# Performance work log

Measured on AMD Instinct MI355X. Metric: run time of the kernel, lower is better.

Reference implementation:

```python
import jax, jax.numpy as jnp
import numpy as np


def setup_inputs() -> dict:
    key = jax.random.key(0)
    kq, kk, kv, km, kb = jax.random.split(key, 5)
    B, H, S, D = 4, 16, 2048, 64
    Q = jax.random.normal(kq, (B, H, S, D), dtype=jnp.float32)
    K = jax.random.normal(kk, (B, H, S, D), dtype=jnp.float32)
    V = jax.random.normal(kv, (B, H, S, D), dtype=jnp.float32)
    # key-padding style mask, broadcasts over query dim; 0 -> masked
    mask = jax.random.randint(km, (B, 1, 1, S), 0, 2, dtype=jnp.int32)
    attn_bias = jax.random.normal(kb, (1, H, S, S), dtype=jnp.float32)
    return {"Q": Q, "K": K, "V": V, "mask": mask, "attn_bias": attn_bias}


def reference(Q, K, V, mask, attn_bias):
    d_k = Q.shape[-1]
    scale = 1.0 / jnp.sqrt(jnp.asarray(d_k, Q.dtype))
    # [B,H,Sq,Sk] scores
    scores = jnp.einsum("bhqd,bhkd->bhqk", Q, K) * scale
    scores = scores + attn_bias
    scores = jnp.where(mask == 0, jnp.asarray(-1e9, scores.dtype), scores)
    attn = jax.nn.softmax(scores, axis=-1)
    # dropout is identity in eval/reference mode
    output = jnp.einsum("bhqk,bhkd->bhqd", attn, V)
    return output, attn
```

## Files before the change

### kernel.cpp

```cpp
#include <hip/hip_runtime.h>

#define NB 4
#define NH 16
#define NS 2048
#define ND 64
#define PST 2052

typedef __attribute__((ext_vector_type(8))) short short8;
typedef __attribute__((ext_vector_type(4))) short short4v;
typedef __attribute__((ext_vector_type(4))) float floatx4;
typedef __attribute__((ext_vector_type(2))) float floatx2;

__device__ __forceinline__ unsigned short f2bf(float f) {
  unsigned u = __builtin_bit_cast(unsigned, f);
  u = (u + 0x7FFFu + ((u >> 16) & 1u)) >> 16;
  return (unsigned short)u;
}
__device__ __forceinline__ float bf2f(unsigned short s) {
  unsigned u = ((unsigned)s) << 16;
  return __builtin_bit_cast(float, u);
}

__global__ __launch_bounds__(256) void prep_k_kernel(const float* __restrict__ K,
                                                     unsigned short* __restrict__ kb) {
  size_t i = ((size_t)blockIdx.x * 256 + threadIdx.x) * 4;
  floatx4 v = *(const floatx4*)(K + i);
  unsigned long long o = 0;
  o |= (unsigned long long)f2bf(v[0]);
  o |= (unsigned long long)f2bf(v[1]) << 16;
  o |= (unsigned long long)f2bf(v[2]) << 32;
  o |= (unsigned long long)f2bf(v[3]) << 48;
  *(unsigned long long*)(kb + i) = o;
}

__global__ __launch_bounds__(256) void prep_vt_kernel(const float* __restrict__ V,
                                                      unsigned short* __restrict__ vt) {
  __shared__ float tile[64][65];
  int kc = blockIdx.x & 31;
  int bh = blockIdx.x >> 5;
  int k0 = kc * 64;
  const float* src = V + ((size_t)bh * NS + k0) * ND;
  int t = threadIdx.x;
  int r0 = t >> 4;
  int c = (t & 15) * 4;
  for (int rr = 0; rr < 4; ++rr) {
    int r = rr * 16 + r0;
    floatx4 v = *(const floatx4*)(src + (size_t)r * ND + c);
    tile[r][c + 0] = v[0]; tile[r][c + 1] = v[1];
    tile[r][c + 2] = v[2]; tile[r][c + 3] = v[3];
  }
  __syncthreads();
  unsigned short* dst = vt + (size_t)bh * ND * NS + k0;
  for (int i = 0; i < 16; ++i) {
    int lin = i * 256 + t;
    int d = lin >> 6, k = lin & 63;
    dst[(size_t)d * NS + k] = f2bf(tile[k][d]);
  }
}

__global__ __launch_bounds__(1024, 8) void attn_kernel(
    const float* __restrict__ Q,
    const unsigned short* __restrict__ Kb,
    const unsigned short* __restrict__ VT,
    const int* __restrict__ mask,
    const float* __restrict__ bias,
    float* __restrict__ out,
    float* __restrict__ attn) {
  extern __shared__ char smem[];
  unsigned short* P = (unsigned short*)smem;
  float* sums = (float*)(smem + 16 * PST * 2);

  const int bid = blockIdx.x;
  const int b = bid & 3;
  const int qt = (bid >> 2) & 127;
  const int h = bid >> 9;
  const int q0 = qt * 16;

  const int tid = threadIdx.x;
  const int wave = tid >> 6;
  const int lane = tid & 63;
  const int lg = lane >> 4;
  const int lc = lane & 15;
  const int lg4 = lg * 4;
  const int lg8 = lg * 8;

  const size_t bh = (size_t)(b * NH + h);

  short8 aq[2];
  {
    const float* qrow = Q + (bh * NS + (size_t)(q0 + lc)) * ND + lg8;
#pragma unroll
    for (int t = 0; t < 2; ++t) {
      floatx4 f0 = *(const floatx4*)(qrow + t * 32);
      floatx4 f1 = *(const floatx4*)(qrow + t * 32 + 4);
      short8 a;
      a[0] = (short)f2bf(f0[0]); a[1] = (short)f2bf(f0[1]);
      a[2] = (short)f2bf(f0[2]); a[3] = (short)f2bf(f0[3]);
      a[4] = (short)f2bf(f1[0]); a[5] = (short)f2bf(f1[1]);
      a[6] = (short)f2bf(f1[2]); a[7] = (short)f2bf(f1[3]);
      aq[t] = a;
    }
  }

  const unsigned short* kp = Kb + bh * NS * ND + (size_t)lc * ND + lg8;
  const float* bprow = bias + ((size_t)h * NS + (size_t)(q0 + lg4)) * NS + lc;
  const int* mp = mask + b * NS + lc;

  float psum[4] = {0.f, 0.f, 0.f, 0.f};
  const int kb0 = wave * 128;

  short8 kfa[2], kfb[2];
  float bvv[2][4];
  int mvv[2];
  {
    const int k0 = kb0;
    kfa[0] = *(const short8*)(kp + (size_t)k0 * ND);
    kfb[0] = *(const short8*)(kp + (size_t)k0 * ND + 32);
    mvv[0] = mp[k0];
#pragma unroll
    for (int r = 0; r < 4; ++r) bvv[0][r] = bprow[(size_t)r * NS + k0];
  }
#pragma unroll
  for (int it = 0; it < 8; ++it) {
    const int cur = it & 1, nxt = cur ^ 1;
    if (it < 7) {
      const int k1 = kb0 + (it + 1) * 16;
      kfa[nxt] = *(const short8*)(kp + (size_t)k1 * ND);
      kfb[nxt] = *(const short8*)(kp + (size_t)k1 * ND + 32);
      mvv[nxt] = mp[k1];
#pragma unroll
      for (int r = 0; r < 4; ++r) bvv[nxt][r] = bprow[(size_t)r * NS + k1];
    }
    const int k0 = kb0 + it * 16;
    floatx4 c = {0.f, 0.f, 0.f, 0.f};
    c = __builtin_amdgcn_mfma_f32_16x16x32_bf16(aq[0], kfa[cur], c, 0, 0, 0);
    c = __builtin_amdgcn_mfma_f32_16x16x32_bf16(aq[1], kfb[cur], c, 0, 0, 0);
#pragma unroll
    for (int r = 0; r < 4; ++r) {
      float s = c[r] * 0.125f + bvv[cur][r];
      float p = mvv[cur] ? __expf(s) : 0.f;
      psum[r] += p;
      P[(lg4 + r) * PST + k0 + lc] = f2bf(p);
    }
  }

#pragma unroll
  for (int r = 0; r < 4; ++r) {
    float v = psum[r];
    v += __shfl_xor(v, 1);
    v += __shfl_xor(v, 2);
    v += __shfl_xor(v, 4);
    v += __shfl_xor(v, 8);
    if (lc == 0) sums[wave * 16 + lg4 + r] = v;
  }
  __syncthreads();

  {
    const int row = wave;
    float tot = 0.f;
#pragma unroll
    for (int w = 0; w < 16; ++w) tot += sums[w * 16 + row];
    const float inv = 1.f / tot;
    float* arow = attn + (bh * NS + (size_t)(q0 + row)) * NS;
    const unsigned short* prow = P + row * PST;
#pragma unroll
    for (int it = 0; it < 8; ++it) {
      const int col = it * 256 + lane * 4;
      short4v pv = *(const short4v*)(prow + col);
      floatx4 f;
      f[0] = bf2f((unsigned short)pv[0]) * inv;
      f[1] = bf2f((unsigned short)pv[1]) * inv;
      f[2] = bf2f((unsigned short)pv[2]) * inv;
      f[3] = bf2f((unsigned short)pv[3]) * inv;
      __builtin_nontemporal_store(f, (floatx4*)(arow + col));
    }
  }

  floatx4 o[4];
#pragma unroll
  for (int dt = 0; dt < 4; ++dt) o[dt] = (floatx4){0.f, 0.f, 0.f, 0.f};

  const unsigned short* vp = VT + bh * (size_t)ND * NS + (size_t)lc * NS + lg8;
#pragma unroll
  for (int it = 0; it < 4; ++it) {
    const int k0 = kb0 + it * 32;
    const unsigned short* pr = P + lc * PST + k0 + lg8;
    short4v lo = *(const short4v*)pr;
    short4v hi = *(const short4v*)(pr + 4);
    short8 pa = __builtin_shufflevector(lo, hi, 0, 1, 2, 3, 4, 5, 6, 7);
#pragma unroll
    for (int dt = 0; dt < 4; ++dt) {
      short8 bb = *(const short8*)(vp + (size_t)(dt * 16) * NS + k0);
      o[dt] = __builtin_amdgcn_mfma_f32_16x16x32_bf16(pa, bb, o[dt], 0, 0, 0);
    }
  }
  __syncthreads();

  float* Ored = (float*)smem;
#pragma unroll
  for (int dt = 0; dt < 4; ++dt)
#pragma unroll
    for (int r = 0; r < 4; ++r)
      Ored[((size_t)wave * 16 + lg4 + r) * 64 + dt * 16 + lc] = o[dt][r];
  __syncthreads();

  {
    const int q = tid >> 6;
    const int col = tid & 63;
    float acc = 0.f;
#pragma unroll
    for (int w = 0; w < 16; ++w) acc += Ored[((size_t)w * 16 + q) * 64 + col];
    float tot = 0.f;
#pragma unroll
    for (int w = 0; w < 16; ++w) tot += sums[w * 16 + q];
    const float inv = 1.f / tot;
    __builtin_nontemporal_store(acc * inv, out + (bh * NS + (size_t)(q0 + q)) * ND + col);
  }
}

extern "C" void kernel_launch(void* const* d_in, const int* in_sizes, int n_in,
                              void* d_out, int out_size, void* d_ws, size_t ws_size,
                              hipStream_t stream) {
  const float* Q = (const float*)d_in[0];
  const float* K = (const float*)d_in[1];
  const float* V = (const float*)d_in[2];
  const int* mask = (const int*)d_in[3];
  const float* bias = (const float*)d_in[4];

  float* out = (float*)d_out;
  float* attn = out + (size_t)NB * NH * NS * ND;

  unsigned short* kb = (unsigned short*)d_ws;
  unsigned short* vt = kb + (size_t)NB * NH * NS * ND;

  const int lds_bytes = 16 * PST * 2 + 16 * 16 * 4;
  (void)hipFuncSetAttribute((const void*)attn_kernel,
                            hipFuncAttributeMaxDynamicSharedMemorySize, lds_bytes);

  prep_k_kernel<<<(NB * NH * NS * ND) / (256 * 4), 256, 0, stream>>>(K, kb);
  prep_vt_kernel<<<NB * NH * (NS / 64), 256, 0, stream>>>(V, vt);
  attn_kernel<<<NB * NH * (NS / 16), 1024, lds_bytes, stream>>>(Q, kb, vt, mask, bias, out, attn);
}
```

Before: 738.8 us.

## Split attention into row-sum and output passes with bf16 bias and async LDS staging

Replaces the single attention kernel with a pipeline of prep kernels and two main kernels. Mask is packed into bitmasks, bias is converted once to bf16 in an MFMA-friendly layout, and a sum_kernel computes softmax denominators. attn_kernel then recomputes the scores, writes normalized attn directly, and does P·V via register shuffles instead of an LDS P buffer. K and V tiles are staged through LDS with global_load_lds double-buffering, and blocks are remapped for locality. This trades recomputing QK^T and an extra bias conversion pass for removing the large per-block P buffer and using fewer, larger tiles, and bias is now rounded to bf16 before being added to the scores.

Result: faster. 693.0 us (-6.2%).

```diff
diff --git a/kernel.cpp b/kernel.cpp
--- a/kernel.cpp
+++ b/kernel.cpp
@@ -4,21 +4,30 @@
 #define NH 16
 #define NS 2048
 #define ND 64
-#define PST 2052
 
 typedef __attribute__((ext_vector_type(8))) short short8;
-typedef __attribute__((ext_vector_type(4))) short short4v;
 typedef __attribute__((ext_vector_type(4))) float floatx4;
-typedef __attribute__((ext_vector_type(2))) float floatx2;
+typedef __attribute__((ext_vector_type(4))) int intx4;
+typedef __attribute__((ext_vector_type(4))) unsigned uintx4;
+
+#define MFMA __builtin_amdgcn_mfma_f32_16x16x32_bf16
+#define WAITV(N) asm volatile("s_waitcnt vmcnt(" #N ")" ::: "memory")
+#define WAITL asm volatile("s_waitcnt lgkmcnt(0)" ::: "memory")
+#define SBAR __builtin_amdgcn_sched_barrier(0)
 
 __device__ __forceinline__ unsigned short f2bf(float f) {
   unsigned u = __builtin_bit_cast(unsigned, f);
   u = (u + 0x7FFFu + ((u >> 16) & 1u)) >> 16;
   return (unsigned short)u;
 }
-__device__ __forceinline__ float bf2f(unsigned short s) {
-  unsigned u = ((unsigned)s) << 16;
+__device__ __forceinline__ float bf2f(unsigned u16) {
+  unsigned u = u16 << 16;
   return __builtin_bit_cast(float, u);
+}
+__device__ __forceinline__ void gload16(const void* g, void* l) {
+  __builtin_amdgcn_global_load_lds(
+      (const __attribute__((address_space(1))) unsigned int*)g,
+      (__attribute__((address_space(3))) unsigned int*)l, 16, 0, 0);
 }
 
 __global__ __launch_bounds__(256) void prep_k_kernel(const float* __restrict__ K,
@@ -58,163 +67,384 @@
   }
 }
 
-__global__ __launch_bounds__(1024, 8) void attn_kernel(
-    const float* __restrict__ Q,
-    const unsigned short* __restrict__ Kb,
-    const unsigned short* __restrict__ VT,
-    const int* __restrict__ mask,
-    const float* __restrict__ bias,
-    float* __restrict__ out,
-    float* __restrict__ attn) {
+__global__ __launch_bounds__(256) void prep_mask_kernel(const int* __restrict__ mask,
+                                                        unsigned* __restrict__ mb) {
+  int t = blockIdx.x * 256 + threadIdx.x;
+  const int* mp = mask + t * 32;
+  unsigned w = 0;
+#pragma unroll
+  for (int i = 0; i < 32; ++i) w |= (mp[i] != 0 ? 1u : 0u) << i;
+  mb[t] = w;
+}
+
+__global__ __launch_bounds__(256) void prep_bias_kernel(const float* __restrict__ bias,
+                                                        unsigned short* __restrict__ bb) {
+  int blk = blockIdx.x;
+  int t = threadIdx.x;
+  int qf = t >> 6, lane = t & 63;
+  int lg = lane >> 4, lc = lane & 15;
+  int Wg = blk & 63;
+  int hq = blk >> 6;
+  int qt = hq & 31, h = hq >> 5;
+  int row = qt * 64 + qf * 16 + lc;
+  int col = Wg * 32 + lg * 4;
+  const float* src = bias + ((size_t)h * NS + row) * NS + col;
+  floatx4 f0 = *(const floatx4*)(src);
+  floatx4 f1 = *(const floatx4*)(src + 16);
+  uintx4 o;
+  o[0] = (unsigned)f2bf(f0[0]) | ((unsigned)f2bf(f0[1]) << 16);
+  o[1] = (unsigned)f2bf(f0[2]) | ((unsigned)f2bf(f0[3]) << 16);
+  o[2] = (unsigned)f2bf(f1[0]) | ((unsigned)f2bf(f1[1]) << 16);
+  o[3] = (unsigned)f2bf(f1[2]) | ((unsigned)f2bf(f1[3]) << 16);
+  *(uintx4*)(bb + ((size_t)blk * 4 + qf) * 512 + lane * 8) = o;
+}
+
+__device__ __forceinline__ void load_aq(const float* __restrict__ Q, size_t bh,
+                                        int q0, int lc, int lg8,
+                                        short8* aq0, short8* aq1) {
+#pragma unroll
+  for (int qf = 0; qf < 4; ++qf) {
+    const float* qrow = Q + (bh * NS + (size_t)(q0 + qf * 16 + lc)) * ND + lg8;
+    floatx4 f0 = *(const floatx4*)(qrow);
+    floatx4 f1 = *(const floatx4*)(qrow + 4);
+    floatx4 f2 = *(const floatx4*)(qrow + 32);
+    floatx4 f3 = *(const floatx4*)(qrow + 36);
+    short8 a0, a1;
+#pragma unroll
+    for (int j = 0; j < 4; ++j) {
+      a0[j] = (short)f2bf(f0[j] * 0.125f);
+      a0[4 + j] = (short)f2bf(f1[j] * 0.125f);
+      a1[j] = (short)f2bf(f2[j] * 0.125f);
+      a1[4 + j] = (short)f2bf(f3[j] * 0.125f);
+    }
+    aq0[qf] = a0; aq1[qf] = a1;
+  }
+}
+
+__global__ void __attribute__((amdgpu_flat_work_group_size(256, 256)))
+sum_kernel(const float* __restrict__ Q, const unsigned short* __restrict__ Kb,
+           const unsigned* __restrict__ maskbits, const unsigned short* __restrict__ bb,
+           float* __restrict__ rs) {
+  __shared__ float sums[4][4][16];
   extern __shared__ char smem[];
-  unsigned short* P = (unsigned short*)smem;
-  float* sums = (float*)(smem + 16 * PST * 2);
-
-  const int bid = blockIdx.x;
+
+  const int bid0 = blockIdx.x;
+  const int bid = (bid0 & 7) * 256 + (bid0 >> 3);
   const int b = bid & 3;
-  const int qt = (bid >> 2) & 127;
-  const int h = bid >> 9;
-  const int q0 = qt * 16;
+  const int qt = (bid >> 2) & 31;
+  const int h = bid >> 7;
+  const int q0 = qt * 64;
 
   const int tid = threadIdx.x;
   const int wave = tid >> 6;
   const int lane = tid & 63;
-  const int lg = lane >> 4;
-  const int lc = lane & 15;
-  const int lg4 = lg * 4;
-  const int lg8 = lg * 8;
-
+  const int lg = lane >> 4, lc = lane & 15;
+  const int lg4 = lg * 4, lg8 = lg * 8;
   const size_t bh = (size_t)(b * NH + h);
 
-  short8 aq[2];
+  __shared__ char kstage_[4][8192];
+  char* kstage = kstage_[wave];
+
+  short8 aq0[4], aq1[4];
+  load_aq(Q, bh, q0, lc, lg8, aq0, aq1);
+
+  const int ksb = wave * 512;
+  intx4 mva, mvb, mvc, mvd;
   {
-    const float* qrow = Q + (bh * NS + (size_t)(q0 + lc)) * ND + lg8;
-#pragma unroll
-    for (int t = 0; t < 2; ++t) {
-      floatx4 f0 = *(const floatx4*)(qrow + t * 32);
-      floatx4 f1 = *(const floatx4*)(qrow + t * 32 + 4);
-      short8 a;
-      a[0] = (short)f2bf(f0[0]); a[1] = (short)f2bf(f0[1]);
-      a[2] = (short)f2bf(f0[2]); a[3] = (short)f2bf(f0[3]);
-      a[4] = (short)f2bf(f1[0]); a[5] = (short)f2bf(f1[1]);
-      a[6] = (short)f2bf(f1[2]); a[7] = (short)f2bf(f1[3]);
-      aq[t] = a;
+    const intx4* mp = (const intx4*)(maskbits + b * 64 + wave * 16);
+    mva = mp[0]; mvb = mp[1]; mvc = mp[2]; mvd = mp[3];
+  }
+  const int kj = (lane & 7) ^ (lane >> 3);
+  const unsigned short* kRowPtr = Kb + bh * NS * ND + (size_t)(lane >> 3) * ND + kj * 8;
+  const unsigned short* bpw = bb + ((size_t)(h * 32 + qt) * 64 + wave * 16) * 2048;
+  const int lc128 = lc * 128;
+  const int kRd0 = ((lg ^ (lc & 7)) * 16);
+  const int kRd1 = (((4 + lg) ^ (lc & 7)) * 16);
+
+  float psum[4] = {0.f, 0.f, 0.f, 0.f};
+  uintx4 bP0[4], bP1[4];
+
+  WAITV(0);
+
+#define KISS1(W, S) {                                                     \
+    const int k0_ = ksb + (W) * 32;                                       \
+    const unsigned short* ks_ = kRowPtr + (size_t)k0_ * ND;               \
+    char* kd_ = kstage + (S) * 4096;                                      \
+    gload16(ks_, kd_); gload16(ks_ + 8 * ND, kd_ + 1024);                 \
+    gload16(ks_ + 16 * ND, kd_ + 2048); gload16(ks_ + 24 * ND, kd_ + 3072); }
+
+#define BL1(W, P) {                                                       \
+    asm volatile("global_load_dwordx4 %0, %1, off" : "=v"(bP##P[0])       \
+                 : "v"(bpw + (size_t)(W) * 2048 + 0 * 512 + lane * 8) : "memory"); \
+    asm volatile("global_load_dwordx4 %0, %1, off" : "=v"(bP##P[1])       \
+                 : "v"(bpw + (size_t)(W) * 2048 + 1 * 512 + lane * 8) : "memory"); \
+    asm volatile("global_load_dwordx4 %0, %1, off" : "=v"(bP##P[2])       \
+                 : "v"(bpw + (size_t)(W) * 2048 + 2 * 512 + lane * 8) : "memory"); \
+    asm volatile("global_load_dwordx4 %0, %1, off" : "=v"(bP##P[3])       \
+                 : "v"(bpw + (size_t)(W) * 2048 + 3 * 512 + lane * 8) : "memory"); }
+
+#define SUB1(W, S, P, NW, MW) {                                           \
+    WAITV(NW); SBAR;                                                      \
+    const char* kb_ = kstage + (S) * 4096;                                \
+    short8 kA0 = *(const short8*)(kb_ + lc128 + kRd0);                    \
+    short8 kB0 = *(const short8*)(kb_ + lc128 + kRd1);                    \
+    short8 kA1 = *(const short8*)(kb_ + 2048 + lc128 + kRd0);             \
+    short8 kB1 = *(const short8*)(kb_ + 2048 + lc128 + kRd1);             \
+    _Pragma("unroll")                                                     \
+    for (int qf = 0; qf < 4; ++qf) {                                      \
+      uintx4 bv = bP##P[qf];                                              \
+      floatx4 c0, c1;                                                     \
+      c0[0] = bf2f(bv[0] & 0xffffu); c0[1] = bf2f(bv[0] >> 16);           \
+      c0[2] = bf2f(bv[1] & 0xffffu); c0[3] = bf2f(bv[1] >> 16);           \
+      c1[0] = bf2f(bv[2] & 0xffffu); c1[1] = bf2f(bv[2] >> 16);           \
+      c1[2] = bf2f(bv[3] & 0xffffu); c1[3] = bf2f(bv[3] >> 16);           \
+      c0 = MFMA(kA0, aq0[qf], c0, 0, 0, 0);                               \
+      c0 = MFMA(kB0, aq1[qf], c0, 0, 0, 0);                               \
+      c1 = MFMA(kA1, aq0[qf], c1, 0, 0, 0);                               \
+      c1 = MFMA(kB1, aq1[qf], c1, 0, 0, 0);                               \
+      unsigned m0 = (MW) >> lg4, m1 = (MW) >> (16 + lg4);                 \
+      float s = 0.f;                                                      \
+      s += (m0 & 1u) ? __expf(c0[0]) : 0.f;                               \
+      s += (m0 & 2u) ? __expf(c0[1]) : 0.f;                               \
+      s += (m0 & 4u) ? __expf(c0[2]) : 0.f;                               \
+      s += (m0 & 8u) ? __expf(c0[3]) : 0.f;                               \
+      s += (m1 & 1u) ? __expf(c1[0]) : 0.f;                               \
+      s += (m1 & 2u) ? __expf(c1[1]) : 0.f;                               \
+      s += (m1 & 4u) ? __expf(c1[2]) : 0.f;                               \
+      s += (m1 & 8u) ? __expf(c1[3]) : 0.f;                               \
+      psum[qf] += s;                                                      \
+    }                                                                     \
+    WAITL; }
+
+  KISS1(0, 0) BL1(0, 0)
+  KISS1(1, 1) BL1(1, 1)
+  SUB1(0, 0, 0, 8, mva[0])  KISS1(2, 0)  BL1(2, 0)
+  SUB1(1, 1, 1, 8, mva[1])  KISS1(3, 1)  BL1(3, 1)
+  SUB1(2, 0, 0, 8, mva[2])  KISS1(4, 0)  BL1(4, 0)
+  SUB1(3, 1, 1, 8, mva[3])  KISS1(5, 1)  BL1(5, 1)
+  SUB1(4, 0, 0, 8, mvb[0])  KISS1(6, 0)  BL1(6, 0)
+  SUB1(5, 1, 1, 8, mvb[1])  KISS1(7, 1)  BL1(7, 1)
+  SUB1(6, 0, 0, 8, mvb[2])  KISS1(8, 0)  BL1(8, 0)
+  SUB1(7, 1, 1, 8, mvb[3])  KISS1(9, 1)  BL1(9, 1)
+  SUB1(8, 0, 0, 8, mvc[0])  KISS1(10, 0) BL1(10, 0)
+  SUB1(9, 1, 1, 8, mvc[1])  KISS1(11, 1) BL1(11, 1)
+  SUB1(10, 0, 0, 8, mvc[2]) KISS1(12, 0) BL1(12, 0)
+  SUB1(11, 1, 1, 8, mvc[3]) KISS1(13, 1) BL1(13, 1)
+  SUB1(12, 0, 0, 8, mvd[0]) KISS1(14, 0) BL1(14, 0)
+  SUB1(13, 1, 1, 8, mvd[1]) KISS1(15, 1) BL1(15, 1)
+  SUB1(14, 0, 0, 8, mvd[2])
+  SUB1(15, 1, 1, 0, mvd[3])
+#undef SUB1
+#undef KISS1
+#undef BL1
+
+#pragma unroll
+  for (int qf = 0; qf < 4; ++qf) {
+    float v = psum[qf];
+    v += __shfl_xor(v, 16);
+    v += __shfl_xor(v, 32);
+    if (lane < 16) sums[wave][qf][lane] = v;
+  }
+  __syncthreads();
+  if (tid < 64) {
+    int qf = tid >> 4, l = tid & 15;
+    float t = sums[0][qf][l] + sums[1][qf][l] + sums[2][qf][l] + sums[3][qf][l];
+    rs[(bh << 11) + q0 + tid] = t;
+  }
+}
+
+__global__ void __attribute__((amdgpu_flat_work_group_size(256, 256),
+                               amdgpu_waves_per_eu(2, 4)))
+attn_kernel(const float* __restrict__ Q, const unsigned short* __restrict__ Kb,
+            const unsigned short* __restrict__ VT, const unsigned* __restrict__ maskbits,
+            const unsigned short* __restrict__ bb, const float* __restrict__ rs,
+            float* __restrict__ out, float* __restrict__ attn) {
+  extern __shared__ char smem[];
+
+  const int bid0 = blockIdx.x;
+  const int bid = (bid0 & 7) * 256 + (bid0 >> 3);
+  const int b = bid & 3;
+  const int qt = (bid >> 2) & 31;
+  const int h = bid >> 7;
+  const int q0 = qt * 64;
+
+  const int tid = threadIdx.x;
+  const int wave = tid >> 6;
+  const int lane = tid & 63;
+  const int lg = lane >> 4, lc = lane & 15;
+  const int lg4 = lg * 4, lg8 = lg * 8;
+  const size_t bh = (size_t)(b * NH + h);
+
+  char* smStage = smem + wave * 16384;
+
+  short8 aq0[4], aq1[4];
+  load_aq(Q, bh, q0, lc, lg8, aq0, aq1);
+  float inv[4];
+#pragma unroll
+  for (int qf = 0; qf < 4; ++qf)
+    inv[qf] = 1.f / rs[(bh << 11) + q0 + qf * 16 + lc];
+
+  const int ksb = wave * 512;
+  intx4 mva, mvb, mvc, mvd;
+  {
+    const intx4* mp = (const intx4*)(maskbits + b * 64 + wave * 16);
+    mva = mp[0]; mvb = mp[1]; mvc = mp[2]; mvd = mp[3];
+  }
+  const int kj = (lane & 7) ^ (lane >> 3);
+  const unsigned short* kRowPtr = Kb + bh * NS * ND + (size_t)(lane >> 3) * ND + kj * 8;
+  const int vj = (lane & 3) ^ ((lane >> 2) & 3);
+  const unsigned short* vRowPtr = VT + bh * (size_t)ND * NS + (size_t)(lane >> 2) * NS + vj * 8;
+  const unsigned short* bpw = bb + ((size_t)(h * 32 + qt) * 64 + wave * 16) * 2048;
+  float* abase = attn + (bh * NS + (size_t)(q0 + lc)) * NS + ksb;
+
+  const int lc128 = lc * 128;
+  const int kRd0 = ((lg ^ (lc & 7)) * 16);
+  const int kRd1 = (((4 + lg) ^ (lc & 7)) * 16);
+  const int vRd = ((lg ^ (lc & 3)) * 16);
+  const bool lo_half = (lg < 2);
+  const bool sndR = (lg == 0) || (lg == 3);
+
+  floatx4 o[4][4];
+#pragma unroll
+  for (int qf = 0; qf < 4; ++qf)
+#pragma unroll
+    for (int dt = 0; dt < 4; ++dt) o[qf][dt] = (floatx4){0.f, 0.f, 0.f, 0.f};
+
+  uintx4 bP0[4], bP1[4];
+  WAITV(0);
+
+#define ISS2(W, S, P) {                                                   \
+    const int k0_ = ksb + (W) * 32;                                       \
+    const unsigned short* vs_ = vRowPtr + k0_;                            \
+    char* vd_ = smStage + 8192 + (S) * 4096;                              \
+    gload16(vs_, vd_); gload16(vs_ + 16 * NS, vd_ + 1024);                \
+    gload16(vs_ + 32 * NS, vd_ + 2048); gload16(vs_ + 48 * NS, vd_ + 3072); \
+    const unsigned short* ks_ = kRowPtr + (size_t)k0_ * ND;               \
+    char* kd_ = smStage + (S) * 4096;                                     \
+    gload16(ks_, kd_); gload16(ks_ + 8 * ND, kd_ + 1024);                 \
+    gload16(ks_ + 16 * ND, kd_ + 2048); gload16(ks_ + 24 * ND, kd_ + 3072); \
+    asm volatile("global_load_dwordx4 %0, %1, off" : "=v"(bP##P[0])       \
+                 : "v"(bpw + (size_t)(W) * 2048 + 0 * 512 + lane * 8) : "memory"); \
+    asm volatile("global_load_dwordx4 %0, %1, off" : "=v"(bP##P[1])       \
+                 : "v"(bpw + (size_t)(W) * 2048 + 1 * 512 + lane * 8) : "memory"); \
+    asm volatile("global_load_dwordx4 %0, %1, off" : "=v"(bP##P[2])       \
+                 : "v"(bpw + (size_t)(W) * 2048 + 2 * 512 + lane * 8) : "memory"); \
+    asm volatile("global_load_dwordx4 %0, %1, off" : "=v"(bP##P[3])       \
+                 : "v"(bpw + (size_t)(W) * 2048 + 3 * 512 + lane * 8) : "memory"); }
+
+#define SUB2(W, S, P, NW, MW) {                                           \
+    WAITV(NW); SBAR;                                                      \
+    const char* kb_ = smStage + (S) * 4096;                               \
+    const char* vb_ = smStage + 8192 + (S) * 4096;                        \
+    short8 kA0 = *(const short8*)(kb_ + lc128 + kRd0);                    \
+    short8 kB0 = *(const short8*)(kb_ + lc128 + kRd1);                    \
+    short8 kA1 = *(const short8*)(kb_ + 2048 + lc128 + kRd0);             \
+    short8 kB1 = *(const short8*)(kb_ + 2048 + lc128 + kRd1);             \
+    short8 vb0 = *(const short8*)(vb_ + (0 * 16 + lc) * 64 + vRd);        \
+    short8 vb1 = *(const short8*)(vb_ + (1 * 16 + lc) * 64 + vRd);        \
+    short8 vb2 = *(const short8*)(vb_ + (2 * 16 + lc) * 64 + vRd);        \
+    short8 vb3 = *(const short8*)(vb_ + (3 * 16 + lc) * 64 + vRd);        \
+    _Pragma("unroll")                                                     \
+    for (int qf = 0; qf < 4; ++qf) {                                      \
+      uintx4 bv = bP##P[qf];                                              \
+      floatx4 c0, c1;                                                     \
+      c0[0] = bf2f(bv[0] & 0xffffu); c0[1] = bf2f(bv[0] >> 16);           \
+      c0[2] = bf2f(bv[1] & 0xffffu); c0[3] = bf2f(bv[1] >> 16);           \
+      c1[0] = bf2f(bv[2] & 0xffffu); c1[1] = bf2f(bv[2] >> 16);           \
+      c1[2] = bf2f(bv[3] & 0xffffu); c1[3] = bf2f(bv[3] >> 16);           \
+      c0 = MFMA(kA0, aq0[qf], c0, 0, 0, 0);                               \
+      c0 = MFMA(kB0, aq1[qf], c0, 0, 0, 0);                               \
+      c1 = MFMA(kA1, aq0[qf], c1, 0, 0, 0);                               \
+      c1 = MFMA(kB1, aq1[qf], c1, 0, 0, 0);                               \
+      unsigned m0 = (MW) >> lg4, m1 = (MW) >> (16 + lg4);                 \
+      const float iv = inv[qf];                                           \
+      float p0 = (m0 & 1u) ? __expf(c0[0]) * iv : 0.f;                    \
+      float p1 = (m0 & 2u) ? __expf(c0[1]) * iv : 0.f;                    \
+      float p2 = (m0 & 4u) ? __expf(c0[2]) * iv : 0.f;                    \
+      float p3 = (m0 & 8u) ? __expf(c0[3]) * iv : 0.f;                    \
+      float p4 = (m1 & 1u) ? __expf(c1[0]) * iv : 0.f;                    \
+      float p5 = (m1 & 2u) ? __expf(c1[1]) * iv : 0.f;                    \
+      float p6 = (m1 & 4u) ? __expf(c1[2]) * iv : 0.f;                    \
+      float p7 = (m1 & 8u) ? __expf(c1[3]) * iv : 0.f;                    \
+      float* ar = abase + (size_t)(qf * 16) * NS + (W) * 32 + lg4;        \
+      floatx4 fa; fa[0] = p0; fa[1] = p1; fa[2] = p2; fa[3] = p3;         \
+      floatx4 fb; fb[0] = p4; fb[1] = p5; fb[2] = p6; fb[3] = p7;         \
+      *(floatx4*)(ar) = fa;                                               \
+      *(floatx4*)(ar + 16) = fb;                                          \
+      unsigned uA0 = (unsigned)f2bf(p0) | ((unsigned)f2bf(p1) << 16);     \
+      unsigned uA1 = (unsigned)f2bf(p2) | ((unsigned)f2bf(p3) << 16);     \
+      unsigned uB0 = (unsigned)f2bf(p4) | ((unsigned)f2bf(p5) << 16);     \
+      unsigned uB1 = (unsigned)f2bf(p6) | ((unsigned)f2bf(p7) << 16);     \
+      unsigned ma = lo_half ? uA0 : uB0;                                  \
+      unsigned mb2 = lo_half ? uA1 : uB1;                                 \
+      unsigned sa = lo_half ? uB0 : uA0;                                  \
+      unsigned sb = lo_half ? uB1 : uA1;                                  \
+      unsigned r1a = __shfl_xor(sa, 32);                                  \
+      unsigned r1b = __shfl_xor(sb, 32);                                  \
+      unsigned s2a = sndR ? r1a : ma;                                     \
+      unsigned s2b = sndR ? r1b : mb2;                                    \
+      unsigned g2a = __shfl_xor(s2a, 16);                                 \
+      unsigned g2b = __shfl_xor(s2b, 16);                                 \
+      uintx4 pw;                                                          \
+      pw[0] = (lg == 0) ? ma : (lg == 2) ? r1a : g2a;                     \
+      pw[1] = (lg == 0) ? mb2 : (lg == 2) ? r1b : g2b;                    \
+      pw[2] = (lg == 1) ? r1a : (lg == 3) ? ma : g2a;                     \
+      pw[3] = (lg == 1) ? r1b : (lg == 3) ? mb2 : g2b;                    \
+      short8 pa = __builtin_bit_cast(short8, pw);                         \
+      o[qf][0] = MFMA(pa, vb0, o[qf][0], 0, 0, 0);                        \
+      o[qf][1] = MFMA(pa, vb1, o[qf][1], 0, 0, 0);                        \
+      o[qf][2] = MFMA(pa, vb2, o[qf][2], 0, 0, 0);                        \
+      o[qf][3] = MFMA(pa, vb3, o[qf][3], 0, 0, 0);                        \
+    }                                                                     \
+    WAITL; }
+
+  ISS2(0, 0, 0)
+  ISS2(1, 1, 1)
+  SUB2(0, 0, 0, 12, mva[0])  ISS2(2, 0, 0)
+  SUB2(1, 1, 1, 20, mva[1])  ISS2(3, 1, 1)
+  SUB2(2, 0, 0, 20, mva[2])  ISS2(4, 0, 0)
+  SUB2(3, 1, 1, 20, mva[3])  ISS2(5, 1, 1)
+  SUB2(4, 0, 0, 20, mvb[0])  ISS2(6, 0, 0)
+  SUB2(5, 1, 1, 20, mvb[1])  ISS2(7, 1, 1)
+  SUB2(6, 0, 0, 20, mvb[2])  ISS2(8, 0, 0)
+  SUB2(7, 1, 1, 20, mvb[3])  ISS2(9, 1, 1)
+  SUB2(8, 0, 0, 20, mvc[0])  ISS2(10, 0, 0)
+  SUB2(9, 1, 1, 20, mvc[1])  ISS2(11, 1, 1)
+  SUB2(10, 0, 0, 20, mvc[2]) ISS2(12, 0, 0)
+  SUB2(11, 1, 1, 20, mvc[3]) ISS2(13, 1, 1)
+  SUB2(12, 0, 0, 20, mvd[0]) ISS2(14, 0, 0)
+  SUB2(13, 1, 1, 20, mvd[1]) ISS2(15, 1, 1)
+  SUB2(14, 0, 0, 20, mvd[2])
+  SUB2(15, 1, 1, 8, mvd[3])
+#undef SUB2
+#undef ISS2
+
+  SBAR;
+  __builtin_amdgcn_s_barrier();
+  SBAR;
+  float (*Ored)[64][68] = (float (*)[64][68])smem;
+#pragma unroll
+  for (int qf = 0; qf < 4; ++qf)
+#pragma unroll
+    for (int dt = 0; dt < 4; ++dt)
+#pragma unroll
+      for (int r = 0; r < 4; ++r)
+        Ored[wave][qf * 16 + lg4 + r][dt * 16 + lc] = o[qf][dt][r];
+  WAITL;
+  SBAR;
+  __builtin_amdgcn_s_barrier();
+  SBAR;
+  {
+    const int row = tid >> 2;
+    const int cb = (tid & 3) * 16;
+    float* orow = out + (bh * NS + (size_t)(q0 + row)) * ND + cb;
+#pragma unroll
+    for (int k = 0; k < 4; ++k) {
+      floatx4 acc = {0.f, 0.f, 0.f, 0.f};
+#pragma unroll
+      for (int w = 0; w < 4; ++w) acc += *(const floatx4*)&Ored[w][row][cb + k * 4];
+      __builtin_nontemporal_store(acc, (floatx4*)(orow + k * 4));
     }
-  }
-
-  const unsigned short* kp = Kb + bh * NS * ND + (size_t)lc * ND + lg8;
-  const float* bprow = bias + ((size_t)h * NS + (size_t)(q0 + lg4)) * NS + lc;
-  const int* mp = mask + b * NS + lc;
-
-  float psum[4] = {0.f, 0.f, 0.f, 0.f};
-  const int kb0 = wave * 128;
-
-  short8 kfa[2], kfb[2];
-  float bvv[2][4];
-  int mvv[2];
-  {
-    const int k0 = kb0;
-    kfa[0] = *(const short8*)(kp + (size_t)k0 * ND);
-    kfb[0] = *(const short8*)(kp + (size_t)k0 * ND + 32);
-    mvv[0] = mp[k0];
-#pragma unroll
-    for (int r = 0; r < 4; ++r) bvv[0][r] = bprow[(size_t)r * NS + k0];
-  }
-#pragma unroll
-  for (int it = 0; it < 8; ++it) {
-    const int cur = it & 1, nxt = cur ^ 1;
-    if (it < 7) {
-      const int k1 = kb0 + (it + 1) * 16;
-      kfa[nxt] = *(const short8*)(kp + (size_t)k1 * ND);
-      kfb[nxt] = *(const short8*)(kp + (size_t)k1 * ND + 32);
-      mvv[nxt] = mp[k1];
-#pragma unroll
-      for (int r = 0; r < 4; ++r) bvv[nxt][r] = bprow[(size_t)r * NS + k1];
-    }
-    const int k0 = kb0 + it * 16;
-    floatx4 c = {0.f, 0.f, 0.f, 0.f};
-    c = __builtin_amdgcn_mfma_f32_16x16x32_bf16(aq[0], kfa[cur], c, 0, 0, 0);
-    c = __builtin_amdgcn_mfma_f32_16x16x32_bf16(aq[1], kfb[cur], c, 0, 0, 0);
-#pragma unroll
-    for (int r = 0; r < 4; ++r) {
-      float s = c[r] * 0.125f + bvv[cur][r];
-      float p = mvv[cur] ? __expf(s) : 0.f;
-      psum[r] += p;
-      P[(lg4 + r) * PST + k0 + lc] = f2bf(p);
-    }
-  }
-
-#pragma unroll
-  for (int r = 0; r < 4; ++r) {
-    float v = psum[r];
-    v += __shfl_xor(v, 1);
-    v += __shfl_xor(v, 2);
-    v += __shfl_xor(v, 4);
-    v += __shfl_xor(v, 8);
-    if (lc == 0) sums[wave * 16 + lg4 + r] = v;
-  }
-  __syncthreads();
-
-  {
-    const int row = wave;
-    float tot = 0.f;
-#pragma unroll
-    for (int w = 0; w < 16; ++w) tot += sums[w * 16 + row];
-    const float inv = 1.f / tot;
-    float* arow = attn + (bh * NS + (size_t)(q0 + row)) * NS;
-    const unsigned short* prow = P + row * PST;
-#pragma unroll
-    for (int it = 0; it < 8; ++it) {
-      const int col = it * 256 + lane * 4;
-      short4v pv = *(const short4v*)(prow + col);
-      floatx4 f;
-      f[0] = bf2f((unsigned short)pv[0]) * inv;
-      f[1] = bf2f((unsigned short)pv[1]) * inv;
-      f[2] = bf2f((unsigned short)pv[2]) * inv;
-      f[3] = bf2f((unsigned short)pv[3]) * inv;
-      __builtin_nontemporal_store(f, (floatx4*)(arow + col));
-    }
-  }
-
-  floatx4 o[4];
-#pragma unroll
-  for (int dt = 0; dt < 4; ++dt) o[dt] = (floatx4){0.f, 0.f, 0.f, 0.f};
-
-  const unsigned short* vp = VT + bh * (size_t)ND * NS + (size_t)lc * NS + lg8;
-#pragma unroll
-  for (int it = 0; it < 4; ++it) {
-    const int k0 = kb0 + it * 32;
-    const unsigned short* pr = P + lc * PST + k0 + lg8;
-    short4v lo = *(const short4v*)pr;
-    short4v hi = *(const short4v*)(pr + 4);
-    short8 pa = __builtin_shufflevector(lo, hi, 0, 1, 2, 3, 4, 5, 6, 7);
-#pragma unroll
-    for (int dt = 0; dt < 4; ++dt) {
-      short8 bb = *(const short8*)(vp + (size_t)(dt * 16) * NS + k0);
-      o[dt] = __builtin_amdgcn_mfma_f32_16x16x32_bf16(pa, bb, o[dt], 0, 0, 0);
-    }
-  }
-  __syncthreads();
-
-  float* Ored = (float*)smem;
-#pragma unroll
-  for (int dt = 0; dt < 4; ++dt)
-#pragma unroll
-    for (int r = 0; r < 4; ++r)
-      Ored[((size_t)wave * 16 + lg4 + r) * 64 + dt * 16 + lc] = o[dt][r];
-  __syncthreads();
-
-  {
-    const int q = tid >> 6;
-    const int col = tid & 63;
-    float acc = 0.f;
-#pragma unroll
-    for (int w = 0; w < 16; ++w) acc += Ored[((size_t)w * 16 + q) * 64 + col];
-    float tot = 0.f;
-#pragma unroll
-    for (int w = 0; w < 16; ++w) tot += sums[w * 16 + q];
-    const float inv = 1.f / tot;
-    __builtin_nontemporal_store(acc * inv, out + (bh * NS + (size_t)(q0 + q)) * ND + col);
   }
 }
 
@@ -230,14 +460,20 @@
   float* out = (float*)d_out;
   float* attn = out + (size_t)NB * NH * NS * ND;
 
-  unsigned short* kb = (unsigned short*)d_ws;
+  unsigned short* bbuf = (unsigned short*)d_ws;
+  unsigned short* kb = bbuf + (size_t)NH * NS * NS;
   unsigned short* vt = kb + (size_t)NB * NH * NS * ND;
-
-  const int lds_bytes = 16 * PST * 2 + 16 * 16 * 4;
+  float* rs = (float*)(vt + (size_t)NB * NH * NS * ND);
+  unsigned* mb = (unsigned*)(rs + (size_t)NB * NH * NS);
+
+  const int lds2 = 69632;
   (void)hipFuncSetAttribute((const void*)attn_kernel,
-                            hipFuncAttributeMaxDynamicSharedMemorySize, lds_bytes);
+                            hipFuncAttributeMaxDynamicSharedMemorySize, lds2);
 
   prep_k_kernel<<<(NB * NH * NS * ND) / (256 * 4), 256, 0, stream>>>(K, kb);
   prep_vt_kernel<<<NB * NH * (NS / 64), 256, 0, stream>>>(V, vt);
-  attn_kernel<<<NB * NH * (NS / 16), 1024, lds_bytes, stream>>>(Q, kb, vt, mask, bias, out, attn);
-}
+  prep_mask_kernel<<<1, 256, 0, stream>>>(mask, mb);
+  prep_bias_kernel<<<NH * 32 * 64, 256, 0, stream>>>(bias, bbuf);
+  sum_kernel<<<NB * NH * (NS / 64), 256, 0, stream>>>(Q, kb, mb, bbuf, rs);
+  attn_kernel<<<NB * NH * (NS / 64), 256, lds2, stream>>>(Q, kb, vt, mb, bbuf, rs, out, attn);
+}
```
